# Kernel optimization log

Measured on AMD Instinct MI355X. Metric: run time of the kernel, lower is better.

Reference implementation:

```python
import jax, jax.numpy as jnp
import numpy as np

A = 5          # num anchors
C = 80         # num classes
STRIDE = 16    # network stride
THRESH = 0.6
OBJ_SCALE = 5.0
NOOBJ_SCALE = 1.0
COORD_SCALE = 1.0
CLASS_SCALE = 1.0


def setup_inputs() -> dict:
    key = jax.random.key(0)
    k1, k2, k3, k4 = jax.random.split(key, 4)
    B, H, W, N = 16, 64, 64, 50
    output = jax.random.normal(k1, (B, A * (5 + C), H, W), dtype=jnp.float32)
    cls_id = jax.random.randint(k2, (B, N, 1), 0, C).astype(jnp.float32)
    cxcy = jax.random.uniform(k3, (B, N, 2), dtype=jnp.float32) * (W * STRIDE)
    wh = jax.random.uniform(k4, (B, N, 2), dtype=jnp.float32) * 290.0 + 10.0
    target = jnp.concatenate([cls_id, cxcy, wh], axis=-1)  # (B, N, 5)
    anchors = jnp.array([[18.3, 21.6], [60.0, 66.0], [106.8, 175.5],
                         [252.2, 112.9], [312.7, 293.4]], dtype=jnp.float32)
    return {"output": output, "target": target, "anchors": anchors}


def _iou(g, p):
    # g: (B, N, 4), p: (B, M, 4), boxes in [cx, cy, w, h]
    gx1, gy1 = g[..., 0] - g[..., 2] / 2, g[..., 1] - g[..., 3] / 2
    gx2, gy2 = g[..., 0] + g[..., 2] / 2, g[..., 1] + g[..., 3] / 2
    px1, py1 = p[..., 0] - p[..., 2] / 2, p[..., 1] - p[..., 3] / 2
    px2, py2 = p[..., 0] + p[..., 2] / 2, p[..., 1] + p[..., 3] / 2
    ix1 = jnp.maximum(gx1[:, :, None], px1[:, None, :])
    iy1 = jnp.maximum(gy1[:, :, None], py1[:, None, :])
    ix2 = jnp.minimum(gx2[:, :, None], px2[:, None, :])
    iy2 = jnp.minimum(gy2[:, :, None], py2[:, None, :])
    inter = jnp.clip(ix2 - ix1, 0) * jnp.clip(iy2 - iy1, 0)
    g_area = (gx2 - gx1) * (gy2 - gy1)
    p_area = (px2 - px1) * (py2 - py1)
    union = g_area[:, :, None] + p_area[:, None, :] - inter + 1e-6
    return inter / union  # (B, N, M)


def reference(output, target, anchors):
    B, _, H, W = output.shape
    out = output.reshape(B, A, 5 + C, H, W).transpose(0, 1, 3, 4, 2)  # (B,A,H,W,5+C)
    coord = out[..., :4]
    conf = out[..., 4]
    cls_logits = out[..., 5:]

    gx = jnp.arange(W, dtype=output.dtype)
    gy = jnp.arange(H, dtype=output.dtype)
    px = (jax.nn.sigmoid(coord[..., 0]) + gx[None, None, None, :]) * STRIDE
    py = (jax.nn.sigmoid(coord[..., 1]) + gy[None, None, :, None]) * STRIDE
    pw = jnp.exp(coord[..., 2]) * anchors[:, 0][None, :, None, None]
    ph = jnp.exp(coord[..., 3]) * anchors[:, 1][None, :, None, None]
    pred_boxes = jnp.stack([px, py, pw, ph], axis=-1).reshape(B, -1, 4)  # (B, A*H*W, 4)

    gt_boxes = target[..., 1:]  # (B, N, 4)
    gt_cls = target[..., 0]     # (B, N)

    iou = _iou(gt_boxes, pred_boxes)          # (B, N, M)
    best_iou = iou.max(axis=1)                # (B, M)
    best_idx = iou.argmax(axis=1)             # (B, M)

    mask = (best_iou > THRESH).reshape(B, A, H, W)
    mask_f = mask.astype(output.dtype)
    conf_mask = jnp.where(mask, OBJ_SCALE, NOOBJ_SCALE).astype(output.dtype)

    tcoord = jnp.take_along_axis(gt_boxes, best_idx[..., None], axis=1)  # (B, M, 4)
    tcoord = tcoord.reshape(B, A, H, W, 4) * mask_f[..., None]
    tcls = jnp.take_along_axis(gt_cls, best_idx, axis=1).reshape(B, A, H, W)
    tcls_idx = (tcls * mask_f).astype(jnp.int32)
    tconf = mask_f

    cm = mask_f[..., None]
    coord_loss = COORD_SCALE * jnp.sum((coord * cm - tcoord * cm) ** 2)
    conf_loss = jnp.sum((conf * conf_mask - tconf * conf_mask) ** 2)
    logp = jax.nn.log_softmax(cls_logits, axis=-1)
    nll = -jnp.take_along_axis(logp, tcls_idx[..., None], axis=-1)[..., 0]
    cls_loss = CLASS_SCALE * jnp.sum(jnp.where(mask, nll, 0.0))

    return coord_loss + conf_loss + cls_loss
```

## Files before the change

kernel.cpp:

```cpp
#include <hip/hip_runtime.h>

#define A_   5
#define C_   80
#define BB   16
#define HH   64
#define WW   64
#define NN   50
#define CH   (5 + C_)
#define HW   (HH * WW)
#define STRIDE_F 16.0f
#define THRESH_F 0.6f

__global__ void zero_out_kernel(float* out) { out[0] = 0.0f; }

__global__ __launch_bounds__(256)
void region_loss_kernel(const float* __restrict__ out4d,
                        const float* __restrict__ target,
                        const float* __restrict__ anchors,
                        float* __restrict__ loss)
{
    __shared__ float g_x1[NN], g_y1[NN], g_x2[NN], g_y2[NN], g_area[NN];
    __shared__ float g_cx[NN], g_cy[NN], g_w[NN], g_h[NN], g_cls[NN];
    __shared__ float wave_sum[4];

    const int bid = blockIdx.x;
    const int h4  = bid & 15;
    const int a   = (bid >> 4) % A_;
    const int b   = bid / (A_ * 16);

    const int tid = threadIdx.x;
    const int w   = tid & 63;
    const int h   = (h4 << 2) + (tid >> 6);

    if (tid < NN) {
        const float* t = target + ((size_t)b * NN + tid) * 5;
        float cls = t[0], cx = t[1], cy = t[2], gw = t[3], gh = t[4];
        g_cls[tid]  = cls;
        g_cx[tid]   = cx;  g_cy[tid] = cy;  g_w[tid] = gw;  g_h[tid] = gh;
        g_x1[tid]   = cx - gw * 0.5f;  g_y1[tid] = cy - gh * 0.5f;
        g_x2[tid]   = cx + gw * 0.5f;  g_y2[tid] = cy + gh * 0.5f;
        g_area[tid] = gw * gh;
    }
    __syncthreads();

    const float* base = out4d + (size_t)(b * (A_ * CH) + a * CH) * HW + h * WW + w;

    const float x0 = base[0 * HW];
    const float x1 = base[1 * HW];
    const float x2 = base[2 * HW];
    const float x3 = base[3 * HW];
    const float cf = base[4 * HW];

    const float aw = anchors[a * 2 + 0];
    const float ah = anchors[a * 2 + 1];

    const float px = (1.0f / (1.0f + __expf(-x0)) + (float)w) * STRIDE_F;
    const float py = (1.0f / (1.0f + __expf(-x1)) + (float)h) * STRIDE_F;
    const float pw = __expf(x2) * aw;
    const float ph = __expf(x3) * ah;
    const float px1 = px - pw * 0.5f, py1 = py - ph * 0.5f;
    const float px2 = px + pw * 0.5f, py2 = py + ph * 0.5f;
    const float parea = pw * ph;

    float best_inter = 0.0f, best_union = 1.0f;
    int best_n = 0;
    for (int n = 0; n < NN; ++n) {
        float ix1 = fmaxf(g_x1[n], px1);
        float iy1 = fmaxf(g_y1[n], py1);
        float ix2 = fminf(g_x2[n], px2);
        float iy2 = fminf(g_y2[n], py2);
        float iw  = fmaxf(ix2 - ix1, 0.0f);
        float ih  = fmaxf(iy2 - iy1, 0.0f);
        float inter = iw * ih;
        float uni   = g_area[n] + parea - inter + 1e-6f;
        if (inter * best_union > best_inter * uni) {
            best_inter = inter; best_union = uni; best_n = n;
        }
    }
    const bool mask = best_inter > THRESH_F * best_union;

    float local;
    if (mask) {
        float d0 = x0 - g_cx[best_n];
        float d1 = x1 - g_cy[best_n];
        float d2 = x2 - g_w[best_n];
        float d3 = x3 - g_h[best_n];
        float cd = 5.0f * cf - 5.0f;
        local = d0*d0 + d1*d1 + d2*d2 + d3*d3 + cd*cd;
    } else {
        local = cf * cf;
    }

    const unsigned long long any_mask = __ballot(mask);
    if (any_mask != 0ull) {
        const int tcls = mask ? (int)g_cls[best_n] : 0;
        float m = -1e30f, s = 0.0f, xt = 0.0f;
        #pragma unroll 4
        for (int c = 0; c < C_; ++c) {
            float x  = base[(5 + c) * HW];
            float nm = fmaxf(m, x);
            s = s * __expf(m - nm) + __expf(x - nm);
            m = nm;
            if (c == tcls) xt = x;
        }
        float lse = m + __logf(s);
        if (mask) local += lse - xt;
    }

    for (int off = 32; off > 0; off >>= 1)
        local += __shfl_down(local, off);
    if ((tid & 63) == 0) wave_sum[tid >> 6] = local;
    __syncthreads();
    if (tid == 0)
        atomicAdd(loss, wave_sum[0] + wave_sum[1] + wave_sum[2] + wave_sum[3]);
}

extern "C" void kernel_launch(void* const* d_in, const int* in_sizes, int n_in,
                              void* d_out, int out_size, void* d_ws, size_t ws_size,
                              hipStream_t stream) {
    const float* output  = (const float*)d_in[0];
    const float* target  = (const float*)d_in[1];
    const float* anchors = (const float*)d_in[2];
    float* loss = (float*)d_out;

    zero_out_kernel<<<1, 1, 0, stream>>>(loss);

    const int grid = BB * A_ * (HH / 4);
    region_loss_kernel<<<grid, 256, 0, stream>>>(output, target, anchors, loss);
}
```

Baseline: 163.0 us.

## Vectorize IoU over four cells per thread, remap class pass, replace atomics with partials

Each thread now loads float4 vectors and evaluates IoU for four adjacent cells, so every shared-memory ground-truth box read is reused four times. Mask and class info are staged in shared memory, and the class log-sum-exp is recomputed per row in coalesced wave layout. That pass uses a plain four-way exp sum instead of the running-max form, which could overflow for large logits. The atomic accumulation and zeroing kernel are replaced by per-block partial sums plus a single finalize kernel.

Measured after the change: 180.0 us. 10.4% more time.

```diff
diff --git a/kernel.cpp b/kernel.cpp
--- a/kernel.cpp
+++ b/kernel.cpp
@@ -8,111 +8,157 @@
 #define NN   50
 #define CH   (5 + C_)
 #define HW   (HH * WW)
+#define ROWS 8
+#define NBLK (BB * A_ * (HH / ROWS))
 #define STRIDE_F 16.0f
-#define THRESH_F 0.6f
 
-__global__ void zero_out_kernel(float* out) { out[0] = 0.0f; }
-
-__global__ __launch_bounds__(256)
-void region_loss_kernel(const float* __restrict__ out4d,
-                        const float* __restrict__ target,
-                        const float* __restrict__ anchors,
-                        float* __restrict__ loss)
+__global__ __launch_bounds__(128)
+void region_loss_main(const float* __restrict__ out4d,
+                      const float* __restrict__ target,
+                      const float* __restrict__ anchors,
+                      float* __restrict__ partial)
 {
-    __shared__ float g_x1[NN], g_y1[NN], g_x2[NN], g_y2[NN], g_area[NN];
-    __shared__ float g_cx[NN], g_cy[NN], g_w[NN], g_h[NN], g_cls[NN];
-    __shared__ float wave_sum[4];
+    __shared__ float4 g_box[NN];
+    __shared__ float  g_area[NN];
+    __shared__ unsigned int pinfo[ROWS * WW];
+    __shared__ float wave_sum[2];
 
     const int bid = blockIdx.x;
-    const int h4  = bid & 15;
-    const int a   = (bid >> 4) % A_;
-    const int b   = bid / (A_ * 16);
+    const int hb  = bid & 7;
+    const int a   = (bid >> 3) % A_;
+    const int b   = bid / (A_ * 8);
+    const int h0  = hb * ROWS;
 
-    const int tid = threadIdx.x;
-    const int w   = tid & 63;
-    const int h   = (h4 << 2) + (tid >> 6);
+    const int tid  = threadIdx.x;
+    const int lane = tid & 63;
+    const int wv   = tid >> 6;
 
     if (tid < NN) {
         const float* t = target + ((size_t)b * NN + tid) * 5;
-        float cls = t[0], cx = t[1], cy = t[2], gw = t[3], gh = t[4];
-        g_cls[tid]  = cls;
-        g_cx[tid]   = cx;  g_cy[tid] = cy;  g_w[tid] = gw;  g_h[tid] = gh;
-        g_x1[tid]   = cx - gw * 0.5f;  g_y1[tid] = cy - gh * 0.5f;
-        g_x2[tid]   = cx + gw * 0.5f;  g_y2[tid] = cy + gh * 0.5f;
+        float cx = t[1], cy = t[2], gw = t[3], gh = t[4];
+        g_box[tid]  = make_float4(cx - 0.5f * gw, cy - 0.5f * gh,
+                                  cx + 0.5f * gw, cy + 0.5f * gh);
         g_area[tid] = gw * gh;
     }
     __syncthreads();
 
-    const float* base = out4d + (size_t)(b * (A_ * CH) + a * CH) * HW + h * WW + w;
+    const int wg = tid & 15;
+    const int hr = tid >> 4;
+    const int h  = h0 + hr;
+    const size_t plane = ((size_t)b * A_ + a) * CH * HW;
+    const float* base = out4d + plane + (size_t)h * WW + wg * 4;
 
-    const float x0 = base[0 * HW];
-    const float x1 = base[1 * HW];
-    const float x2 = base[2 * HW];
-    const float x3 = base[3 * HW];
-    const float cf = base[4 * HW];
+    const float4 v0 = *(const float4*)(base + 0 * HW);
+    const float4 v1 = *(const float4*)(base + 1 * HW);
+    const float4 v2 = *(const float4*)(base + 2 * HW);
+    const float4 v3 = *(const float4*)(base + 3 * HW);
+    const float4 vc = *(const float4*)(base + 4 * HW);
 
     const float aw = anchors[a * 2 + 0];
     const float ah = anchors[a * 2 + 1];
 
-    const float px = (1.0f / (1.0f + __expf(-x0)) + (float)w) * STRIDE_F;
-    const float py = (1.0f / (1.0f + __expf(-x1)) + (float)h) * STRIDE_F;
-    const float pw = __expf(x2) * aw;
-    const float ph = __expf(x3) * ah;
-    const float px1 = px - pw * 0.5f, py1 = py - ph * 0.5f;
-    const float px2 = px + pw * 0.5f, py2 = py + ph * 0.5f;
-    const float parea = pw * ph;
+    const float X0[4] = {v0.x, v0.y, v0.z, v0.w};
+    const float X1[4] = {v1.x, v1.y, v1.z, v1.w};
+    const float X2[4] = {v2.x, v2.y, v2.z, v2.w};
+    const float X3[4] = {v3.x, v3.y, v3.z, v3.w};
+    const float CF[4] = {vc.x, vc.y, vc.z, vc.w};
 
-    float best_inter = 0.0f, best_union = 1.0f;
-    int best_n = 0;
+    float PX1[4], PY1[4], PX2[4], PY2[4], PAREA[4];
+    #pragma unroll
+    for (int j = 0; j < 4; ++j) {
+        float w_f = (float)(wg * 4 + j);
+        float px = (1.0f / (1.0f + __expf(-X0[j])) + w_f) * STRIDE_F;
+        float py = (1.0f / (1.0f + __expf(-X1[j])) + (float)h) * STRIDE_F;
+        float pw = __expf(X2[j]) * aw;
+        float ph = __expf(X3[j]) * ah;
+        PX1[j] = px - 0.5f * pw;  PY1[j] = py - 0.5f * ph;
+        PX2[j] = px + 0.5f * pw;  PY2[j] = py + 0.5f * ph;
+        PAREA[j] = pw * ph;
+    }
+
+    float bi[4] = {0, 0, 0, 0};
+    float bu[4] = {1, 1, 1, 1};
+    int   bn[4] = {0, 0, 0, 0};
     for (int n = 0; n < NN; ++n) {
-        float ix1 = fmaxf(g_x1[n], px1);
-        float iy1 = fmaxf(g_y1[n], py1);
-        float ix2 = fminf(g_x2[n], px2);
-        float iy2 = fminf(g_y2[n], py2);
-        float iw  = fmaxf(ix2 - ix1, 0.0f);
-        float ih  = fmaxf(iy2 - iy1, 0.0f);
-        float inter = iw * ih;
-        float uni   = g_area[n] + parea - inter + 1e-6f;
-        if (inter * best_union > best_inter * uni) {
-            best_inter = inter; best_union = uni; best_n = n;
+        const float4 gb = g_box[n];
+        const float  ga = g_area[n];
+        #pragma unroll
+        for (int j = 0; j < 4; ++j) {
+            float ix1 = fmaxf(gb.x, PX1[j]);
+            float iy1 = fmaxf(gb.y, PY1[j]);
+            float ix2 = fminf(gb.z, PX2[j]);
+            float iy2 = fminf(gb.w, PY2[j]);
+            float iw  = fmaxf(ix2 - ix1, 0.0f);
+            float ih  = fmaxf(iy2 - iy1, 0.0f);
+            float inter = iw * ih;
+            float uni   = ga + PAREA[j] - inter + 1e-6f;
+            if (inter * bu[j] > bi[j] * uni) {
+                bi[j] = inter; bu[j] = uni; bn[j] = n;
+            }
         }
     }
-    const bool mask = best_inter > THRESH_F * best_union;
 
-    float local;
-    if (mask) {
-        float d0 = x0 - g_cx[best_n];
-        float d1 = x1 - g_cy[best_n];
-        float d2 = x2 - g_w[best_n];
-        float d3 = x3 - g_h[best_n];
-        float cd = 5.0f * cf - 5.0f;
-        local = d0*d0 + d1*d1 + d2*d2 + d3*d3 + cd*cd;
-    } else {
-        local = cf * cf;
+    float local = 0.0f;
+    #pragma unroll
+    for (int j = 0; j < 4; ++j) {
+        const bool mask = bi[j] > 0.6f * bu[j];
+        const float cf = CF[j];
+        unsigned int info = 0u;
+        if (mask) {
+            const float* t = target + ((size_t)b * NN + bn[j]) * 5;
+            float d0 = X0[j] - t[1];
+            float d1 = X1[j] - t[2];
+            float d2 = X2[j] - t[3];
+            float d3 = X3[j] - t[4];
+            float cd = 5.0f * cf - 5.0f;
+            local += d0*d0 + d1*d1 + d2*d2 + d3*d3 + cd*cd;
+            info = 0x80000000u | (unsigned int)(int)t[0];
+        } else {
+            local += cf * cf;
+        }
+        pinfo[hr * WW + wg * 4 + j] = info;
     }
+    __syncthreads();
 
-    const unsigned long long any_mask = __ballot(mask);
-    if (any_mask != 0ull) {
-        const int tcls = mask ? (int)g_cls[best_n] : 0;
-        float m = -1e30f, s = 0.0f, xt = 0.0f;
-        #pragma unroll 4
-        for (int c = 0; c < C_; ++c) {
-            float x  = base[(5 + c) * HW];
-            float nm = fmaxf(m, x);
-            s = s * __expf(m - nm) + __expf(x - nm);
-            m = nm;
-            if (c == tcls) xt = x;
+    for (int r = 0; r < 4; ++r) {
+        const int row = wv * 4 + r;
+        const unsigned int info = pinfo[row * WW + lane];
+        const bool m = (info & 0x80000000u) != 0u;
+        if (__ballot(m) != 0ull) {
+            const float* cb = out4d + plane + (size_t)(5) * HW
+                            + (size_t)(h0 + row) * WW + lane;
+            float s0 = 0.f, s1 = 0.f, s2 = 0.f, s3 = 0.f;
+            #pragma unroll 4
+            for (int c = 0; c < C_; c += 4) {
+                s0 += __expf(cb[(c + 0) * HW]);
+                s1 += __expf(cb[(c + 1) * HW]);
+                s2 += __expf(cb[(c + 2) * HW]);
+                s3 += __expf(cb[(c + 3) * HW]);
+            }
+            if (m) {
+                const int tcls = (int)(info & 0xFFu);
+                const float xt = cb[tcls * HW];
+                local += __logf((s0 + s1) + (s2 + s3)) - xt;
+            }
         }
-        float lse = m + __logf(s);
-        if (mask) local += lse - xt;
     }
 
     for (int off = 32; off > 0; off >>= 1)
         local += __shfl_down(local, off);
-    if ((tid & 63) == 0) wave_sum[tid >> 6] = local;
+    if (lane == 0) wave_sum[wv] = local;
     __syncthreads();
-    if (tid == 0)
-        atomicAdd(loss, wave_sum[0] + wave_sum[1] + wave_sum[2] + wave_sum[3]);
+    if (tid == 0) partial[bid] = wave_sum[0] + wave_sum[1];
+}
+
+__global__ __launch_bounds__(64)
+void region_loss_finalize(const float* __restrict__ partial, float* __restrict__ out)
+{
+    float s = 0.0f;
+    for (int i = threadIdx.x; i < NBLK; i += 64)
+        s += partial[i];
+    for (int off = 32; off > 0; off >>= 1)
+        s += __shfl_down(s, off);
+    if (threadIdx.x == 0) out[0] = s;
 }
 
 extern "C" void kernel_launch(void* const* d_in, const int* in_sizes, int n_in,
@@ -121,10 +167,9 @@
     const float* output  = (const float*)d_in[0];
     const float* target  = (const float*)d_in[1];
     const float* anchors = (const float*)d_in[2];
-    float* loss = (float*)d_out;
+    float* loss    = (float*)d_out;
+    float* partial = (float*)d_ws;
 
-    zero_out_kernel<<<1, 1, 0, stream>>>(loss);
-
-    const int grid = BB * A_ * (HH / 4);
-    region_loss_kernel<<<grid, 256, 0, stream>>>(output, target, anchors, loss);
+    region_loss_main<<<NBLK, 128, 0, stream>>>(output, target, anchors, partial);
+    region_loss_finalize<<<1, 64, 0, stream>>>(partial, loss);
 }
```

## Split region loss into prep, per-wave main, and deterministic finalize kernels

Applied to the files above, without the earlier changes.

Precomputes ground-truth box corners and areas in a small prep kernel, so the main kernel reads them from global memory (float4) instead of staging them through shared memory with a block barrier. The main kernel now uses 128-thread blocks with one wave per row, writes one partial sum per wave, and a single-block finalize kernel replaces the atomicAdd. The class log-sum-exp drops the running-max rescaling and sums exp directly with four accumulators, which removes dependent work but risks overflow for large logits. It also adds two extra kernel launches and a workspace round trip.

New measurement: 171.5 us. 1.05x slower.

```diff
diff --git a/kernel.cpp b/kernel.cpp
--- a/kernel.cpp
+++ b/kernel.cpp
@@ -9,41 +9,45 @@
 #define CH   (5 + C_)
 #define HW   (HH * WW)
 #define STRIDE_F 16.0f
-#define THRESH_F 0.6f
 
-__global__ void zero_out_kernel(float* out) { out[0] = 0.0f; }
+#define NWAVES (BB * A_ * HH)
+#define NBLK   (NWAVES / 2)
+
+#define GBOX_OFF   0
+#define GAREA_OFF  (BB * NN * 4)
+#define PART_OFF   (GAREA_OFF + BB * NN)
 
 __global__ __launch_bounds__(256)
-void region_loss_kernel(const float* __restrict__ out4d,
-                        const float* __restrict__ target,
-                        const float* __restrict__ anchors,
-                        float* __restrict__ loss)
+void region_prep(const float* __restrict__ target, float* __restrict__ ws)
 {
-    __shared__ float g_x1[NN], g_y1[NN], g_x2[NN], g_y2[NN], g_area[NN];
-    __shared__ float g_cx[NN], g_cy[NN], g_w[NN], g_h[NN], g_cls[NN];
-    __shared__ float wave_sum[4];
+    int i = threadIdx.x + blockIdx.x * 256;
+    if (i < BB * NN) {
+        const float* t = target + (size_t)i * 5;
+        float cx = t[1], cy = t[2], gw = t[3], gh = t[4];
+        float4* gbox = (float4*)(ws + GBOX_OFF);
+        gbox[i] = make_float4(cx - 0.5f * gw, cy - 0.5f * gh,
+                              cx + 0.5f * gw, cy + 0.5f * gh);
+        ws[GAREA_OFF + i] = gw * gh;
+    }
+}
 
-    const int bid = blockIdx.x;
-    const int h4  = bid & 15;
-    const int a   = (bid >> 4) % A_;
-    const int b   = bid / (A_ * 16);
+__global__ __launch_bounds__(128)
+void region_loss_main(const float* __restrict__ out4d,
+                      const float* __restrict__ target,
+                      const float* __restrict__ anchors,
+                      const float* __restrict__ ws,
+                      float* __restrict__ partial)
+{
+    const int tid  = threadIdx.x;
+    const int lane = tid & 63;
+    const int wv   = tid >> 6;
+    const int gwid = blockIdx.x * 2 + wv;
+    const int h    = gwid & 63;
+    const int a    = (gwid >> 6) % A_;
+    const int b    = gwid / (A_ * HH);
 
-    const int tid = threadIdx.x;
-    const int w   = tid & 63;
-    const int h   = (h4 << 2) + (tid >> 6);
-
-    if (tid < NN) {
-        const float* t = target + ((size_t)b * NN + tid) * 5;
-        float cls = t[0], cx = t[1], cy = t[2], gw = t[3], gh = t[4];
-        g_cls[tid]  = cls;
-        g_cx[tid]   = cx;  g_cy[tid] = cy;  g_w[tid] = gw;  g_h[tid] = gh;
-        g_x1[tid]   = cx - gw * 0.5f;  g_y1[tid] = cy - gh * 0.5f;
-        g_x2[tid]   = cx + gw * 0.5f;  g_y2[tid] = cy + gh * 0.5f;
-        g_area[tid] = gw * gh;
-    }
-    __syncthreads();
-
-    const float* base = out4d + (size_t)(b * (A_ * CH) + a * CH) * HW + h * WW + w;
+    const size_t plane = ((size_t)b * A_ + a) * CH * HW;
+    const float* base  = out4d + plane + (size_t)h * WW + lane;
 
     const float x0 = base[0 * HW];
     const float x1 = base[1 * HW];
@@ -54,65 +58,86 @@
     const float aw = anchors[a * 2 + 0];
     const float ah = anchors[a * 2 + 1];
 
-    const float px = (1.0f / (1.0f + __expf(-x0)) + (float)w) * STRIDE_F;
+    const float px = (1.0f / (1.0f + __expf(-x0)) + (float)lane) * STRIDE_F;
     const float py = (1.0f / (1.0f + __expf(-x1)) + (float)h) * STRIDE_F;
     const float pw = __expf(x2) * aw;
     const float ph = __expf(x3) * ah;
-    const float px1 = px - pw * 0.5f, py1 = py - ph * 0.5f;
-    const float px2 = px + pw * 0.5f, py2 = py + ph * 0.5f;
+    const float px1 = px - 0.5f * pw, py1 = py - 0.5f * ph;
+    const float px2 = px + 0.5f * pw, py2 = py + 0.5f * ph;
     const float parea = pw * ph;
 
-    float best_inter = 0.0f, best_union = 1.0f;
-    int best_n = 0;
+    const float4* gb_b = (const float4*)(ws + GBOX_OFF) + b * NN;
+    const float*  ga_b = ws + GAREA_OFF + b * NN;
+
+    float bi = 0.0f, bu = 1.0f;
+    int   bn = 0;
+    #pragma unroll 2
     for (int n = 0; n < NN; ++n) {
-        float ix1 = fmaxf(g_x1[n], px1);
-        float iy1 = fmaxf(g_y1[n], py1);
-        float ix2 = fminf(g_x2[n], px2);
-        float iy2 = fminf(g_y2[n], py2);
+        const float4 gb = gb_b[n];
+        const float  ga = ga_b[n];
+        float ix1 = fmaxf(gb.x, px1);
+        float iy1 = fmaxf(gb.y, py1);
+        float ix2 = fminf(gb.z, px2);
+        float iy2 = fminf(gb.w, py2);
         float iw  = fmaxf(ix2 - ix1, 0.0f);
         float ih  = fmaxf(iy2 - iy1, 0.0f);
         float inter = iw * ih;
-        float uni   = g_area[n] + parea - inter + 1e-6f;
-        if (inter * best_union > best_inter * uni) {
-            best_inter = inter; best_union = uni; best_n = n;
+        float uni   = ga + parea - inter + 1e-6f;
+        if (inter * bu > bi * uni) {
+            bi = inter; bu = uni; bn = n;
         }
     }
-    const bool mask = best_inter > THRESH_F * best_union;
+    const bool mask = bi > 0.6f * bu;
 
     float local;
+    int tcls = 0;
     if (mask) {
-        float d0 = x0 - g_cx[best_n];
-        float d1 = x1 - g_cy[best_n];
-        float d2 = x2 - g_w[best_n];
-        float d3 = x3 - g_h[best_n];
+        const float* t = target + ((size_t)b * NN + bn) * 5;
+        float d0 = x0 - t[1];
+        float d1 = x1 - t[2];
+        float d2 = x2 - t[3];
+        float d3 = x3 - t[4];
         float cd = 5.0f * cf - 5.0f;
         local = d0*d0 + d1*d1 + d2*d2 + d3*d3 + cd*cd;
+        tcls = (int)t[0];
     } else {
         local = cf * cf;
     }
 
-    const unsigned long long any_mask = __ballot(mask);
-    if (any_mask != 0ull) {
-        const int tcls = mask ? (int)g_cls[best_n] : 0;
-        float m = -1e30f, s = 0.0f, xt = 0.0f;
+    if (__ballot(mask) != 0ull) {
+        const float* cb = base + 5 * HW;
+        float s0 = 0.f, s1 = 0.f, s2 = 0.f, s3 = 0.f;
         #pragma unroll 4
-        for (int c = 0; c < C_; ++c) {
-            float x  = base[(5 + c) * HW];
-            float nm = fmaxf(m, x);
-            s = s * __expf(m - nm) + __expf(x - nm);
-            m = nm;
-            if (c == tcls) xt = x;
+        for (int c = 0; c < C_; c += 4) {
+            s0 += __expf(cb[(c + 0) * HW]);
+            s1 += __expf(cb[(c + 1) * HW]);
+            s2 += __expf(cb[(c + 2) * HW]);
+            s3 += __expf(cb[(c + 3) * HW]);
         }
-        float lse = m + __logf(s);
-        if (mask) local += lse - xt;
+        if (mask) {
+            const float xt = cb[tcls * HW];
+            local += __logf((s0 + s1) + (s2 + s3)) - xt;
+        }
     }
 
     for (int off = 32; off > 0; off >>= 1)
         local += __shfl_down(local, off);
-    if ((tid & 63) == 0) wave_sum[tid >> 6] = local;
+    if (lane == 0) partial[gwid] = local;
+}
+
+__global__ __launch_bounds__(256)
+void region_loss_finalize(const float* __restrict__ partial, float* __restrict__ out)
+{
+    __shared__ float wsum[4];
+    const int tid = threadIdx.x;
+    float s = 0.0f;
+    for (int i = tid; i < NWAVES; i += 256)
+        s += partial[i];
+    for (int off = 32; off > 0; off >>= 1)
+        s += __shfl_down(s, off);
+    if ((tid & 63) == 0) wsum[tid >> 6] = s;
     __syncthreads();
-    if (tid == 0)
-        atomicAdd(loss, wave_sum[0] + wave_sum[1] + wave_sum[2] + wave_sum[3]);
+    if (tid == 0) out[0] = wsum[0] + wsum[1] + wsum[2] + wsum[3];
 }
 
 extern "C" void kernel_launch(void* const* d_in, const int* in_sizes, int n_in,
@@ -122,9 +147,10 @@
     const float* target  = (const float*)d_in[1];
     const float* anchors = (const float*)d_in[2];
     float* loss = (float*)d_out;
+    float* ws   = (float*)d_ws;
 
-    zero_out_kernel<<<1, 1, 0, stream>>>(loss);
-
-    const int grid = BB * A_ * (HH / 4);
-    region_loss_kernel<<<grid, 256, 0, stream>>>(output, target, anchors, loss);
+    region_prep<<<(BB * NN + 255) / 256, 256, 0, stream>>>(target, ws);
+    region_loss_main<<<NBLK, 128, 0, stream>>>(output, target, anchors,
+                                               ws, ws + PART_OFF);
+    region_loss_finalize<<<1, 256, 0, stream>>>(ws + PART_OFF, loss);
 }
```
